# Kernel optimization log

Hardware: AMD Instinct MI355X
Metric: run time of the kernel (lower is better)

The kernel has to match this reference:

```python
import jax, jax.numpy as jnp
import numpy as np

B, S, IN_DIM, OUT_DIM = 16, 1024, 1024, 1024
NEG_SLOPE = 0.01  # torch F.leaky_relu default


def setup_inputs() -> dict:
    key = jax.random.key(0)
    ks = jax.random.split(key, 10)
    sc_in = 1.0 / np.sqrt(IN_DIM)
    sc_out = 1.0 / np.sqrt(OUT_DIM)
    return {
        "xs": jax.random.normal(ks[0], (B, S, IN_DIM), dtype=jnp.float32),
        "mask": jax.random.randint(ks[1], (B, S), 0, 2, dtype=jnp.int32),
        "Wk": jax.random.uniform(ks[2], (OUT_DIM, IN_DIM), jnp.float32, -sc_in, sc_in),
        "bk": jax.random.uniform(ks[3], (OUT_DIM,), jnp.float32, -sc_in, sc_in),
        "Wq": jax.random.uniform(ks[4], (OUT_DIM, IN_DIM), jnp.float32, -sc_in, sc_in),
        "bq": jax.random.uniform(ks[5], (OUT_DIM,), jnp.float32, -sc_in, sc_in),
        "Wv": jax.random.uniform(ks[6], (OUT_DIM, IN_DIM), jnp.float32, -sc_in, sc_in),
        "bv": jax.random.uniform(ks[7], (OUT_DIM,), jnp.float32, -sc_in, sc_in),
        "Wlin": jax.random.uniform(ks[8], (OUT_DIM, OUT_DIM), jnp.float32, -sc_out, sc_out),
        "blin": jax.random.uniform(ks[9], (OUT_DIM,), jnp.float32, -sc_out, sc_out),
    }


def reference(xs, mask, Wk, bk, Wq, bq, Wv, bv, Wlin, blin):
    # projections: torch Linear is x @ W.T + b
    K = jnp.einsum('bsi,oi->bso', xs, Wk) + bk  # [B,S,D]
    Q = jnp.einsum('bsi,oi->bso', xs, Wq) + bq  # [B,S,D]
    V = jnp.einsum('bsi,oi->bso', xs, Wv) + bv  # [B,S,D]
    # qk[b,s,e] = sum_d K[b,s,d] * Q[b,e,d]
    qk = jnp.einsum('bsd,bed->bse', K, Q) / xs.shape[-1]
    # mask.repeat(1,S).view(B,S,S) => element [b,i,j] = mask[b,j] (column/key mask)
    qk = jnp.where(mask[:, None, :].astype(bool), qk, -jnp.inf)
    a = jax.nn.softmax(qk, axis=-1)  # [B,S,S]
    # faithful to einsum('bij,bik->bik'): sum a over last axis, scale V elementwise
    attn = jnp.sum(a, axis=-1, keepdims=True) * V  # [B,S,D]
    out = jnp.einsum('bsd,od->bso', attn, Wlin) + blin
    return jnp.where(out >= 0, out, NEG_SLOPE * out)
```

## Files before the change

### kernel.cpp

```cpp
#include <hip/hip_runtime.h>
#include <hip/hip_bf16.h>
#include <stdint.h>


#define M_TOT 16384
#define KDIM  1024
#define NDIM  1024
#define NT    32

typedef __attribute__((ext_vector_type(8))) short bf16x8;
typedef __attribute__((ext_vector_type(4))) float f32x4;
typedef __attribute__((ext_vector_type(4))) unsigned short u16x4;
typedef __attribute__((ext_vector_type(8))) unsigned short u16x8;

static __device__ __forceinline__ unsigned short f2bf(float f) {
    union { float f; unsigned int u; } v; v.f = f;
    unsigned int u = v.u;
    return (unsigned short)((u + 0x7fffu + ((u >> 16) & 1u)) >> 16);
}

static __device__ __forceinline__ void gload16(const void* g, void* l) {
    __builtin_amdgcn_global_load_lds(
        (__attribute__((address_space(1))) void*)(g),
        (__attribute__((address_space(3))) void*)(l), 16, 0, 0);
}

static __device__ __forceinline__ int swz(int p) {
    return p ^ (((p >> 9) & 1) << 5) ^ (((p >> 8) & 1) << 4);
}

__global__ __launch_bounds__(256) void prep0_kernel(
    const float* __restrict__ Wv, const float* __restrict__ Wlin,
    const float* __restrict__ bv, const float* __restrict__ blin,
    unsigned short* __restrict__ Wvt, unsigned short* __restrict__ Wlb,
    float* __restrict__ bcomb) {
    __shared__ float Tl[64 * 65];
    const int bid = blockIdx.x;
    const int t = threadIdx.x;

    if (bid < 256) {
        const int dt = bid >> 4;
        const int it = bid & 15;
        const int r = t >> 2;
        const int c0 = (t & 3) * 16;
        #pragma unroll
        for (int u = 0; u < 4; ++u) {
            float4 v = *(const float4*)&Wv[((size_t)(dt * 64 + r)) * NDIM + it * 64 + c0 + 4 * u];
            Tl[r * 65 + c0 + 4 * u + 0] = v.x;
            Tl[r * 65 + c0 + 4 * u + 1] = v.y;
            Tl[r * 65 + c0 + 4 * u + 2] = v.z;
            Tl[r * 65 + c0 + 4 * u + 3] = v.w;
        }
        __syncthreads();
        const int i = t >> 2;
        const int dq = (t & 3) * 16;
        float v[16];
        #pragma unroll
        for (int u = 0; u < 16; ++u) v[u] = Tl[(dq + u) * 65 + i];
        u16x8 p0 = { f2bf(v[0]), f2bf(v[1]), f2bf(v[2]), f2bf(v[3]),
                     f2bf(v[4]), f2bf(v[5]), f2bf(v[6]), f2bf(v[7]) };
        u16x8 p1 = { f2bf(v[8]), f2bf(v[9]), f2bf(v[10]), f2bf(v[11]),
                     f2bf(v[12]), f2bf(v[13]), f2bf(v[14]), f2bf(v[15]) };
        unsigned short* dst = &Wvt[((size_t)(it * 64 + i)) * KDIM + dt * 64 + dq];
        *(u16x8*)dst = p0;
        *(u16x8*)(dst + 8) = p1;
    } else if (bid < 512) {
        const size_t idx = (((size_t)(bid - 256)) * 256 + t) * 16;
        float4 a = *(const float4*)&Wlin[idx];
        float4 b = *(const float4*)&Wlin[idx + 4];
        float4 c = *(const float4*)&Wlin[idx + 8];
        float4 d = *(const float4*)&Wlin[idx + 12];
        u16x8 p0 = { f2bf(a.x), f2bf(a.y), f2bf(a.z), f2bf(a.w),
                     f2bf(b.x), f2bf(b.y), f2bf(b.z), f2bf(b.w) };
        u16x8 p1 = { f2bf(c.x), f2bf(c.y), f2bf(c.z), f2bf(c.w),
                     f2bf(d.x), f2bf(d.y), f2bf(d.z), f2bf(d.w) };
        *(u16x8*)&Wlb[idx] = p0;
        *(u16x8*)&Wlb[idx + 8] = p1;
    } else {
        const int wave = t >> 6, lane = t & 63;
        const int o = (bid - 512) * 4 + wave;
        float s = 0.f;
        for (int d = lane; d < KDIM; d += 64) s += Wlin[o * KDIM + d] * bv[d];
        #pragma unroll
        for (int off = 32; off > 0; off >>= 1) s += __shfl_down(s, off, 64);
        if (lane == 0) bcomb[o] = s + blin[o];
    }
}

__global__ __launch_bounds__(256) void prep1_kernel(
    const unsigned short* __restrict__ Wlb, const unsigned short* __restrict__ Wvt,
    const float* __restrict__ xs, unsigned short* __restrict__ Wc,
    unsigned short* __restrict__ Xb) {
    __shared__ unsigned short As[128 * 32];
    __shared__ unsigned short Bs[128 * 32];
    const int bid = blockIdx.x;
    const int t = threadIdx.x;

    if (bid >= 64) {
        const size_t base = (((size_t)(bid - 64)) * 256 + t) * 8;
        #pragma unroll
        for (int itr = 0; itr < 4; ++itr) {
            const size_t idx = base + (size_t)itr * (size_t)(2048 * 256 * 8);
            float4 a = *(const float4*)&xs[idx];
            float4 b = *(const float4*)&xs[idx + 4];
            u16x8 p = { f2bf(a.x), f2bf(a.y), f2bf(a.z), f2bf(a.w),
                        f2bf(b.x), f2bf(b.y), f2bf(b.z), f2bf(b.w) };
            *(u16x8*)&Xb[idx] = p;
        }
        return;
    }

    const int nt8 = bid & 7;
    const int mt8 = bid >> 3;
    const int w = t >> 6, l = t & 63;
    const int wr = (w >> 1) * 64, wcc = (w & 1) * 64;
    const int lr = l & 15, lk = l >> 4;

    f32x4 acc[4][4] = {};

    const int srow = t >> 2;
    const int sc8 = (t & 3) * 8;
    const unsigned short* gA = &Wlb[((size_t)(mt8 * 128) + srow) * KDIM + sc8];
    const unsigned short* gB = &Wvt[((size_t)(nt8 * 128) + srow) * KDIM + sc8];
    unsigned short* lA0 = &As[w * 512];
    unsigned short* lB0 = &Bs[w * 512];

    for (int kt = 0; kt < KDIM / 32; ++kt) {
        #pragma unroll
        for (int j = 0; j < 2; ++j) {
            gload16(gA + (size_t)j * 64 * KDIM + kt * 32, lA0 + j * 2048);
            gload16(gB + (size_t)j * 64 * KDIM + kt * 32, lB0 + j * 2048);
        }
        __syncthreads();
        bf16x8 af[4], bfr[4];
        #pragma unroll
        for (int fi = 0; fi < 4; ++fi)
            af[fi] = *(bf16x8*)&As[(wr + fi * 16 + lr) * 32 + lk * 8];
        #pragma unroll
        for (int fj = 0; fj < 4; ++fj)
            bfr[fj] = *(bf16x8*)&Bs[(wcc + fj * 16 + lr) * 32 + lk * 8];
        #pragma unroll
        for (int fi = 0; fi < 4; ++fi)
            #pragma unroll
            for (int fj = 0; fj < 4; ++fj)
                acc[fi][fj] = __builtin_amdgcn_mfma_f32_16x16x32_bf16(
                    af[fi], bfr[fj], acc[fi][fj], 0, 0, 0);
        __syncthreads();
    }

    #pragma unroll
    for (int fi = 0; fi < 4; ++fi)
        #pragma unroll
        for (int fj = 0; fj < 4; ++fj) {
            const int col = nt8 * 128 + wcc + fj * 16 + lr;
            #pragma unroll
            for (int r = 0; r < 4; ++r) {
                const int row = mt8 * 128 + wr + fi * 16 + lk * 4 + r;
                Wc[(size_t)row * KDIM + col] = f2bf(acc[fi][fj][r]);
            }
        }
}

__global__ __launch_bounds__(512, 2) void main_gemm_8p(
    const unsigned short* __restrict__ Xb, const unsigned short* __restrict__ Wc,
    const float* __restrict__ bcomb, float* __restrict__ out) {
    extern __shared__ char lds[];
    const int tid = threadIdx.x;
    const int w = tid >> 6, l = tid & 63;
    const int wm = w >> 2, wn = w & 3;
    const int lr = l & 15, lk = l >> 4;

    const int swzb = ((blockIdx.x & 7) << 5) + (blockIdx.x >> 3);
    const int mt = swzb >> 2, nt = swzb & 3;

    int aoff[8], boff[4];
    #pragma unroll
    for (int fi = 0; fi < 8; ++fi)
        aoff[fi] = swz((wm * 128 + fi * 16 + lr) * 64 + lk * 16);
    #pragma unroll
    for (int fj = 0; fj < 4; ++fj)
        boff[fj] = 16384 + swz((wn * 64 + fj * 16 + lr) * 64 + lk * 16);

    const char* srcA0; const char* srcA1; const char* srcB0; const char* srcB1;
    {
        int q0 = 0 * 8192 + w * 1024 + l * 16, p0 = swz(q0);
        int q1 = 1 * 8192 + w * 1024 + l * 16, p1 = swz(q1);
        srcA0 = (const char*)Xb + ((size_t)(mt * 256 + (p0 >> 6)) * KDIM) * 2 + (p0 & 63);
        srcA1 = (const char*)Xb + ((size_t)(mt * 256 + (p1 >> 6)) * KDIM) * 2 + (p1 & 63);
        srcB0 = (const char*)Wc + ((size_t)(nt * 256 + (p0 >> 6)) * KDIM) * 2 + (p0 & 63);
        srcB1 = (const char*)Wc + ((size_t)(nt * 256 + (p1 >> 6)) * KDIM) * 2 + (p1 & 63);
    }
    const int ldsw = w * 1024;

    f32x4 acc[8][4] = {};

    #pragma unroll
    for (int pt = 0; pt < 3; ++pt) {
        char* bb = lds + pt * 32768;
        gload16(srcA0 + (size_t)pt * 64, bb + ldsw);
        gload16(srcA1 + (size_t)pt * 64, bb + 8192 + ldsw);
        gload16(srcB0 + (size_t)pt * 64, bb + 16384 + ldsw);
        gload16(srcB1 + (size_t)pt * 64, bb + 24576 + ldsw);
    }

#define KTILE(T, STAGE_EN)                                                     \
    do {                                                                       \
        const char* bufp = lds + (size_t)((T) & 3) * 32768;                    \
        char* nb = lds + (size_t)(((T) + 3) & 3) * 32768;                      \
        if (STAGE_EN) {                                                        \
            gload16(srcA0 + (size_t)((T) + 3) * 64, nb + ldsw);                \
            gload16(srcA1 + (size_t)((T) + 3) * 64, nb + 8192 + ldsw);         \
        }                                                                      \
        bf16x8 bfr[4], afr[4];                                                 \
        _Pragma("unroll")                                                      \
        for (int fj = 0; fj < 4; ++fj)                                         \
            bfr[fj] = *(const bf16x8*)(bufp + boff[fj]);                       \
        _Pragma("unroll")                                                      \
        for (int fi = 0; fi < 4; ++fi)                                         \
            afr[fi] = *(const bf16x8*)(bufp + aoff[fi]);                       \
        __builtin_amdgcn_s_barrier();                                          \
        __builtin_amdgcn_s_setprio(1);                                         \
        _Pragma("unroll")                                                      \
        for (int fi = 0; fi < 4; ++fi)                                         \
            _Pragma("unroll")                                                  \
            for (int fj = 0; fj < 4; ++fj)                                     \
                acc[fi][fj] = __builtin_amdgcn_mfma_f32_16x16x32_bf16(         \
                    afr[fi], bfr[fj], acc[fi][fj], 0, 0, 0);                   \
        __builtin_amdgcn_s_setprio(0);                                         \
        __builtin_amdgcn_s_barrier();                                          \
        if (STAGE_EN) {                                                        \
            gload16(srcB0 + (size_t)((T) + 3) * 64, nb + 16384 + ldsw);        \
            gload16(srcB1 + (size_t)((T) + 3) * 64, nb + 24576 + ldsw);        \
        }                                                                      \
        bf16x8 af2[4];                                                         \
        _Pragma("unroll")                                                      \
        for (int fi = 0; fi < 4; ++fi)                                         \
            af2[fi] = *(const bf16x8*)(bufp + aoff[4 + fi]);                   \
        __builtin_amdgcn_s_barrier();                                          \
        __builtin_amdgcn_s_setprio(1);                                         \
        _Pragma("unroll")                                                      \
        for (int fi = 0; fi < 4; ++fi)                                         \
            _Pragma("unroll")                                                  \
            for (int fj = 0; fj < 4; ++fj)                                     \
                acc[4 + fi][fj] = __builtin_amdgcn_mfma_f32_16x16x32_bf16(     \
                    af2[fi], bfr[fj], acc[4 + fi][fj], 0, 0, 0);               \
        __builtin_amdgcn_s_setprio(0);                                         \
    } while (0)

    for (int t = 0; t < NT - 3; ++t) {
        asm volatile("s_waitcnt vmcnt(8)" ::: "memory");
        __builtin_amdgcn_s_barrier();
        KTILE(t, 1);
    }
    asm volatile("s_waitcnt vmcnt(8)" ::: "memory");
    __builtin_amdgcn_s_barrier();
    KTILE(29, 0);
    asm volatile("s_waitcnt vmcnt(4)" ::: "memory");
    __builtin_amdgcn_s_barrier();
    KTILE(30, 0);
    asm volatile("s_waitcnt vmcnt(0)" ::: "memory");
    __builtin_amdgcn_s_barrier();
    KTILE(31, 0);
#undef KTILE

    #pragma unroll
    for (int fi = 0; fi < 8; ++fi)
        #pragma unroll
        for (int fj = 0; fj < 4; ++fj) {
            const int col = nt * 256 + wn * 64 + fj * 16 + lr;
            const float b = bcomb[col];
            #pragma unroll
            for (int r = 0; r < 4; ++r) {
                const int row = mt * 256 + wm * 128 + fi * 16 + lk * 4 + r;
                float v = acc[fi][fj][r] + b;
                out[(size_t)row * NDIM + col] = v >= 0.f ? v : 0.01f * v;
            }
        }
}

__global__ __launch_bounds__(256) void main_gemm_f32(
    const float* __restrict__ X, const unsigned short* __restrict__ Wc,
    const float* __restrict__ bcomb, float* __restrict__ out) {
    __shared__ unsigned short As[128 * 32];
    __shared__ unsigned short Bs[128 * 32];
    const int t = threadIdx.x;
    const int nt = blockIdx.x & 7;
    const int mt = blockIdx.x >> 3;
    const int w = t >> 6, l = t & 63;
    const int wr = (w >> 1) * 64, wcc = (w & 1) * 64;
    const int lr = l & 15, lk = l >> 4;

    f32x4 acc[4][4] = {};

    const int arow = t >> 3;
    const int akq = t & 7;
    const int brow = t >> 2;
    const int bc4 = t & 3;

    for (int kt = 0; kt < KDIM / 32; ++kt) {
        float4 av[4];
        #pragma unroll
        for (int j = 0; j < 4; ++j) {
            const int row = j * 32 + arow;
            av[j] = *(const float4*)&X[(mt * 128 + row) * KDIM + kt * 32 + akq * 4];
        }
        __syncthreads();
        #pragma unroll
        for (int j = 0; j < 4; ++j) {
            const int row = j * 32 + arow;
            u16x4 p = { f2bf(av[j].x), f2bf(av[j].y), f2bf(av[j].z), f2bf(av[j].w) };
            *(u16x4*)&As[row * 32 + akq * 4] = p;
        }
        #pragma unroll
        for (int j = 0; j < 2; ++j) {
            const int row = j * 64 + brow;
            const unsigned short* g = &Wc[(nt * 128 + row) * KDIM + kt * 32 + bc4 * 8];
            unsigned short* ldst = &Bs[(j * 256 + w * 64) * 8];
            gload16(g, ldst);
        }
        __syncthreads();
        bf16x8 af[4], bfr[4];
        #pragma unroll
        for (int fi = 0; fi < 4; ++fi)
            af[fi] = *(bf16x8*)&As[(wr + fi * 16 + lr) * 32 + lk * 8];
        #pragma unroll
        for (int fj = 0; fj < 4; ++fj)
            bfr[fj] = *(bf16x8*)&Bs[(wcc + fj * 16 + lr) * 32 + lk * 8];
        #pragma unroll
        for (int fi = 0; fi < 4; ++fi)
            #pragma unroll
            for (int fj = 0; fj < 4; ++fj)
                acc[fi][fj] = __builtin_amdgcn_mfma_f32_16x16x32_bf16(
                    af[fi], bfr[fj], acc[fi][fj], 0, 0, 0);
    }

    #pragma unroll
    for (int fi = 0; fi < 4; ++fi)
        #pragma unroll
        for (int fj = 0; fj < 4; ++fj) {
            const int col = nt * 128 + wcc + fj * 16 + lr;
            const float b = bcomb[col];
            #pragma unroll
            for (int r = 0; r < 4; ++r) {
                const int row = mt * 128 + wr + fi * 16 + lk * 4 + r;
                float v = acc[fi][fj][r] + b;
                out[row * NDIM + col] = v >= 0.f ? v : 0.01f * v;
            }
        }
}

extern "C" void kernel_launch(void* const* d_in, const int* in_sizes, int n_in,
                              void* d_out, int out_size, void* d_ws, size_t ws_size,
                              hipStream_t stream) {
    const float* xs   = (const float*)d_in[0];
    const float* Wv   = (const float*)d_in[6];
    const float* bv   = (const float*)d_in[7];
    const float* Wlin = (const float*)d_in[8];
    const float* blin = (const float*)d_in[9];

    unsigned short* Wc = (unsigned short*)d_ws;
    float* bcomb = (float*)((char*)d_ws + 2097152);
    unsigned short* Xb = (unsigned short*)((char*)d_ws + 2101248);
    float* out = (float*)d_out;

    unsigned short* Wvt = (unsigned short*)d_out;
    unsigned short* Wlb = (unsigned short*)((char*)d_out + 2097152);

    const size_t NEED = 2101248 + (size_t)M_TOT * KDIM * 2;
    if (ws_size >= NEED) {
        (void)hipFuncSetAttribute((const void*)main_gemm_8p,
                                  hipFuncAttributeMaxDynamicSharedMemorySize,
                                  131072);
        hipLaunchKernelGGL(prep0_kernel, dim3(768), dim3(256), 0, stream,
                           Wv, Wlin, bv, blin, Wvt, Wlb, bcomb);
        hipLaunchKernelGGL(prep1_kernel, dim3(64 + 2048), dim3(256), 0, stream,
                           Wlb, Wvt, xs, Wc, Xb);
        hipLaunchKernelGGL(main_gemm_8p, dim3(256), dim3(512), 131072, stream,
                           Xb, Wc, bcomb, out);
    } else {
        hipLaunchKernelGGL(prep0_kernel, dim3(768), dim3(256), 0, stream,
                           Wv, Wlin, bv, blin, Wvt, Wlb, bcomb);
        hipLaunchKernelGGL(prep1_kernel, dim3(64), dim3(256), 0, stream,
                           Wlb, Wvt, xs, Wc, Xb);
        hipLaunchKernelGGL(main_gemm_f32, dim3((M_TOT / 128) * (NDIM / 128)),
                           dim3(256), 0, stream, xs, Wc, bcomb, out);
    }
}
```

Measured before the change: 83.10 us.

## Fuse fp32-to-bf16 conversion of xs into main GEMM A-tile loading

```diff
diff --git a/kernel.cpp b/kernel.cpp
--- a/kernel.cpp
+++ b/kernel.cpp
@@ -6,7 +6,7 @@
 #define M_TOT 16384
 #define KDIM  1024
 #define NDIM  1024
-#define NT    32
+#define NKT   16
 
 typedef __attribute__((ext_vector_type(8))) short bf16x8;
 typedef __attribute__((ext_vector_type(4))) float f32x4;
@@ -19,14 +19,20 @@
     return (unsigned short)((u + 0x7fffu + ((u >> 16) & 1u)) >> 16);
 }
 
+static __device__ __forceinline__ u16x8 pack8(float4 a, float4 b) {
+    u16x8 p = { f2bf(a.x), f2bf(a.y), f2bf(a.z), f2bf(a.w),
+                f2bf(b.x), f2bf(b.y), f2bf(b.z), f2bf(b.w) };
+    return p;
+}
+
 static __device__ __forceinline__ void gload16(const void* g, void* l) {
     __builtin_amdgcn_global_load_lds(
         (__attribute__((address_space(1))) void*)(g),
         (__attribute__((address_space(3))) void*)(l), 16, 0, 0);
 }
 
-static __device__ __forceinline__ int swz(int p) {
-    return p ^ (((p >> 9) & 1) << 5) ^ (((p >> 8) & 1) << 4);
+static __device__ __forceinline__ int swz128(int p) {
+    return p ^ (((p >> 7) & 7) << 4);
 }
 
 __global__ __launch_bounds__(256) void prep0_kernel(
@@ -70,12 +76,8 @@
         float4 b = *(const float4*)&Wlin[idx + 4];
         float4 c = *(const float4*)&Wlin[idx + 8];
         float4 d = *(const float4*)&Wlin[idx + 12];
-        u16x8 p0 = { f2bf(a.x), f2bf(a.y), f2bf(a.z), f2bf(a.w),
-                     f2bf(b.x), f2bf(b.y), f2bf(b.z), f2bf(b.w) };
-        u16x8 p1 = { f2bf(c.x), f2bf(c.y), f2bf(c.z), f2bf(c.w),
-                     f2bf(d.x), f2bf(d.y), f2bf(d.z), f2bf(d.w) };
-        *(u16x8*)&Wlb[idx] = p0;
-        *(u16x8*)&Wlb[idx + 8] = p1;
+        *(u16x8*)&Wlb[idx] = pack8(a, b);
+        *(u16x8*)&Wlb[idx + 8] = pack8(c, d);
     } else {
         const int wave = t >> 6, lane = t & 63;
         const int o = (bid - 512) * 4 + wave;
@@ -87,82 +89,58 @@
     }
 }
 
-__global__ __launch_bounds__(256) void prep1_kernel(
+__global__ __launch_bounds__(256) void wcomb_kernel(
     const unsigned short* __restrict__ Wlb, const unsigned short* __restrict__ Wvt,
-    const float* __restrict__ xs, unsigned short* __restrict__ Wc,
-    unsigned short* __restrict__ Xb) {
-    __shared__ unsigned short As[128 * 32];
-    __shared__ unsigned short Bs[128 * 32];
-    const int bid = blockIdx.x;
+    unsigned short* __restrict__ Wc) {
+    __shared__ unsigned short As[64 * 32];
+    __shared__ unsigned short Bs[64 * 32];
     const int t = threadIdx.x;
-
-    if (bid >= 64) {
-        const size_t base = (((size_t)(bid - 64)) * 256 + t) * 8;
-        #pragma unroll
-        for (int itr = 0; itr < 4; ++itr) {
-            const size_t idx = base + (size_t)itr * (size_t)(2048 * 256 * 8);
-            float4 a = *(const float4*)&xs[idx];
-            float4 b = *(const float4*)&xs[idx + 4];
-            u16x8 p = { f2bf(a.x), f2bf(a.y), f2bf(a.z), f2bf(a.w),
-                        f2bf(b.x), f2bf(b.y), f2bf(b.z), f2bf(b.w) };
-            *(u16x8*)&Xb[idx] = p;
-        }
-        return;
-    }
-
-    const int nt8 = bid & 7;
-    const int mt8 = bid >> 3;
+    const int ot = blockIdx.x >> 4;
+    const int it = blockIdx.x & 15;
     const int w = t >> 6, l = t & 63;
-    const int wr = (w >> 1) * 64, wcc = (w & 1) * 64;
+    const int wr = (w >> 1) * 32, wc = (w & 1) * 32;
     const int lr = l & 15, lk = l >> 4;
 
-    f32x4 acc[4][4] = {};
-
-    const int srow = t >> 2;
-    const int sc8 = (t & 3) * 8;
-    const unsigned short* gA = &Wlb[((size_t)(mt8 * 128) + srow) * KDIM + sc8];
-    const unsigned short* gB = &Wvt[((size_t)(nt8 * 128) + srow) * KDIM + sc8];
-    unsigned short* lA0 = &As[w * 512];
-    unsigned short* lB0 = &Bs[w * 512];
+    f32x4 acc[2][2] = {};
+
+    const unsigned short* gA = &Wlb[((size_t)(ot * 64 + (t >> 2))) * KDIM + (t & 3) * 8];
+    const unsigned short* gB = &Wvt[((size_t)(it * 64 + (t >> 2))) * KDIM + (t & 3) * 8];
+    unsigned short* lA = &As[w * 512];
+    unsigned short* lB = &Bs[w * 512];
 
     for (int kt = 0; kt < KDIM / 32; ++kt) {
-        #pragma unroll
-        for (int j = 0; j < 2; ++j) {
-            gload16(gA + (size_t)j * 64 * KDIM + kt * 32, lA0 + j * 2048);
-            gload16(gB + (size_t)j * 64 * KDIM + kt * 32, lB0 + j * 2048);
-        }
+        gload16(gA + kt * 32, lA);
+        gload16(gB + kt * 32, lB);
         __syncthreads();
-        bf16x8 af[4], bfr[4];
-        #pragma unroll
-        for (int fi = 0; fi < 4; ++fi)
+        bf16x8 af[2], bfr[2];
+        #pragma unroll
+        for (int fi = 0; fi < 2; ++fi)
             af[fi] = *(bf16x8*)&As[(wr + fi * 16 + lr) * 32 + lk * 8];
         #pragma unroll
-        for (int fj = 0; fj < 4; ++fj)
-            bfr[fj] = *(bf16x8*)&Bs[(wcc + fj * 16 + lr) * 32 + lk * 8];
-        #pragma unroll
-        for (int fi = 0; fi < 4; ++fi)
+        for (int fj = 0; fj < 2; ++fj)
+            bfr[fj] = *(bf16x8*)&Bs[(wc + fj * 16 + lr) * 32 + lk * 8];
+        #pragma unroll
+        for (int fi = 0; fi < 2; ++fi)
             #pragma unroll
-            for (int fj = 0; fj < 4; ++fj)
+            for (int fj = 0; fj < 2; ++fj)
                 acc[fi][fj] = __builtin_amdgcn_mfma_f32_16x16x32_bf16(
                     af[fi], bfr[fj], acc[fi][fj], 0, 0, 0);
         __syncthreads();
     }
-
-    #pragma unroll
-    for (int fi = 0; fi < 4; ++fi)
-        #pragma unroll
-        for (int fj = 0; fj < 4; ++fj) {
-            const int col = nt8 * 128 + wcc + fj * 16 + lr;
+    #pragma unroll
+    for (int fi = 0; fi < 2; ++fi)
+        #pragma unroll
+        for (int fj = 0; fj < 2; ++fj)
             #pragma unroll
             for (int r = 0; r < 4; ++r) {
-                const int row = mt8 * 128 + wr + fi * 16 + lk * 4 + r;
-                Wc[(size_t)row * KDIM + col] = f2bf(acc[fi][fj][r]);
+                const int o = ot * 64 + wr + fi * 16 + lk * 4 + r;
+                const int i = it * 64 + wc + fj * 16 + lr;
+                Wc[(size_t)o * KDIM + i] = f2bf(acc[fi][fj][r]);
             }
-        }
-}
-
-__global__ __launch_bounds__(512, 2) void main_gemm_8p(
-    const unsigned short* __restrict__ Xb, const unsigned short* __restrict__ Wc,
+}
+
+__global__ __launch_bounds__(512, 2) void main_fused(
+    const float* __restrict__ xs, const unsigned short* __restrict__ Wc,
     const float* __restrict__ bcomb, float* __restrict__ out) {
     extern __shared__ char lds[];
     const int tid = threadIdx.x;
@@ -176,92 +154,146 @@
     int aoff[8], boff[4];
     #pragma unroll
     for (int fi = 0; fi < 8; ++fi)
-        aoff[fi] = swz((wm * 128 + fi * 16 + lr) * 64 + lk * 16);
+        aoff[fi] = swz128((wm * 128 + fi * 16 + lr) * 128 + lk * 16);
     #pragma unroll
     for (int fj = 0; fj < 4; ++fj)
-        boff[fj] = 16384 + swz((wn * 64 + fj * 16 + lr) * 64 + lk * 16);
-
-    const char* srcA0; const char* srcA1; const char* srcB0; const char* srcB1;
+        boff[fj] = 32768 + swz128((wn * 64 + fj * 16 + lr) * 128 + lk * 16);
+
+    const float* gA[4];
+    int awr[4];
+    #pragma unroll
+    for (int j = 0; j < 4; ++j) {
+        const int row = j * 64 + (tid >> 3);
+        gA[j] = xs + ((size_t)(mt * 256 + row)) * KDIM + (tid & 7) * 8;
+        awr[j] = swz128(row * 128 + (tid & 7) * 16);
+    }
+    const char* gB[4];
+    #pragma unroll
+    for (int j = 0; j < 4; ++j) {
+        const int q = j * 8192 + w * 1024 + l * 16;
+        const int p = swz128(q);
+        gB[j] = (const char*)Wc + ((size_t)(nt * 256 + (p >> 7))) * 2048 + (p & 127);
+    }
+    const int bofs[4] = { 32768 + w * 1024, 32768 + 8192 + w * 1024,
+                          32768 + 16384 + w * 1024, 32768 + 24576 + w * 1024 };
+
+    f32x4 acc[8][4] = {};
+
     {
-        int q0 = 0 * 8192 + w * 1024 + l * 16, p0 = swz(q0);
-        int q1 = 1 * 8192 + w * 1024 + l * 16, p1 = swz(q1);
-        srcA0 = (const char*)Xb + ((size_t)(mt * 256 + (p0 >> 6)) * KDIM) * 2 + (p0 & 63);
-        srcA1 = (const char*)Xb + ((size_t)(mt * 256 + (p1 >> 6)) * KDIM) * 2 + (p1 & 63);
-        srcB0 = (const char*)Wc + ((size_t)(nt * 256 + (p0 >> 6)) * KDIM) * 2 + (p0 & 63);
-        srcB1 = (const char*)Wc + ((size_t)(nt * 256 + (p1 >> 6)) * KDIM) * 2 + (p1 & 63);
-    }
-    const int ldsw = w * 1024;
-
-    f32x4 acc[8][4] = {};
-
-    #pragma unroll
-    for (int pt = 0; pt < 3; ++pt) {
-        char* bb = lds + pt * 32768;
-        gload16(srcA0 + (size_t)pt * 64, bb + ldsw);
-        gload16(srcA1 + (size_t)pt * 64, bb + 8192 + ldsw);
-        gload16(srcB0 + (size_t)pt * 64, bb + 16384 + ldsw);
-        gload16(srcB1 + (size_t)pt * 64, bb + 24576 + ldsw);
-    }
-
-#define KTILE(T, STAGE_EN)                                                     \
+        float4 av[8];
+        #pragma unroll
+        for (int j = 0; j < 4; ++j) {
+            av[2 * j]     = *(const float4*)(gA[j]);
+            av[2 * j + 1] = *(const float4*)(gA[j] + 4);
+        }
+        #pragma unroll
+        for (int j = 0; j < 4; ++j)
+            gload16(gB[j], lds + bofs[j]);
+        #pragma unroll
+        for (int j = 0; j < 4; ++j)
+            *(u16x8*)(lds + awr[j]) = pack8(av[2 * j], av[2 * j + 1]);
+        asm volatile("s_waitcnt vmcnt(0)" ::: "memory");
+        asm volatile("s_waitcnt lgkmcnt(0)" ::: "memory");
+        __builtin_amdgcn_s_barrier();
+    }
+
+#define MFMA16(ACCI, AF, BF)                                                   \
+    _Pragma("unroll")                                                          \
+    for (int fi = 0; fi < 4; ++fi)                                             \
+        _Pragma("unroll")                                                      \
+        for (int fj = 0; fj < 4; ++fj)                                         \
+            acc[(ACCI) + fi][fj] = __builtin_amdgcn_mfma_f32_16x16x32_bf16(    \
+                (AF)[fi], (BF)[fj], acc[(ACCI) + fi][fj], 0, 0, 0)
+
+#define PH_SYNC()                                                              \
+    __builtin_amdgcn_s_barrier();                                              \
+    asm volatile("s_waitcnt lgkmcnt(0)" ::: "memory");                         \
+    __builtin_amdgcn_sched_barrier(0)
+
+#define ITER(T, SEN)                                                           \
     do {                                                                       \
-        const char* bufp = lds + (size_t)((T) & 3) * 32768;                    \
-        char* nb = lds + (size_t)(((T) + 3) & 3) * 32768;                      \
-        if (STAGE_EN) {                                                        \
-            gload16(srcA0 + (size_t)((T) + 3) * 64, nb + ldsw);                \
-            gload16(srcA1 + (size_t)((T) + 3) * 64, nb + 8192 + ldsw);         \
+        const int cb = ((T) & 1) << 16;                                        \
+        char* cbuf = lds + cb;                                                 \
+        char* nbuf = lds + (cb ^ 65536);                                       \
+        float4 av[8];                                                          \
+        if (SEN) {                                                             \
+            _Pragma("unroll")                                                  \
+            for (int j = 0; j < 4; ++j) {                                      \
+                av[2 * j]     = *(const float4*)(gA[j] + ((T) + 1) * 64);      \
+                av[2 * j + 1] = *(const float4*)(gA[j] + ((T) + 1) * 64 + 4);  \
+            }                                                                  \
+            gload16(gB[0] + ((size_t)(T) + 1) * 128, nbuf + bofs[0]);          \
+            gload16(gB[1] + ((size_t)(T) + 1) * 128, nbuf + bofs[1]);          \
         }                                                                      \
-        bf16x8 bfr[4], afr[4];                                                 \
+                                               \
+        bf16x8 b0[4], a0[4];                                                   \
         _Pragma("unroll")                                                      \
         for (int fj = 0; fj < 4; ++fj)                                         \
-            bfr[fj] = *(const bf16x8*)(bufp + boff[fj]);                       \
+            b0[fj] = *(const bf16x8*)(cbuf + boff[fj]);                        \
         _Pragma("unroll")                                                      \
         for (int fi = 0; fi < 4; ++fi)                                         \
-            afr[fi] = *(const bf16x8*)(bufp + aoff[fi]);                       \
-        __builtin_amdgcn_s_barrier();                                          \
+            a0[fi] = *(const bf16x8*)(cbuf + aoff[fi]);                        \
+        PH_SYNC();                                                             \
         __builtin_amdgcn_s_setprio(1);                                         \
-        _Pragma("unroll")                                                      \
-        for (int fi = 0; fi < 4; ++fi)                                         \
-            _Pragma("unroll")                                                  \
-            for (int fj = 0; fj < 4; ++fj)                                     \
-                acc[fi][fj] = __builtin_amdgcn_mfma_f32_16x16x32_bf16(         \
-                    afr[fi], bfr[fj], acc[fi][fj], 0, 0, 0);                   \
+        MFMA16(0, a0, b0);                                                     \
         __builtin_amdgcn_s_setprio(0);                                         \
         __builtin_amdgcn_s_barrier();                                          \
-        if (STAGE_EN) {                                                        \
-            gload16(srcB0 + (size_t)((T) + 3) * 64, nb + 16384 + ldsw);        \
-            gload16(srcB1 + (size_t)((T) + 3) * 64, nb + 24576 + ldsw);        \
+                    \
+        bf16x8 a1[4];                                                          \
+        _Pragma("unroll")                                                      \
+        for (int fi = 0; fi < 4; ++fi)                                         \
+            a1[fi] = *(const bf16x8*)(cbuf + aoff[4 + fi]);                    \
+        if (SEN) {                                                             \
+            *(u16x8*)(nbuf + awr[0]) = pack8(av[0], av[1]);                    \
+            *(u16x8*)(nbuf + awr[1]) = pack8(av[2], av[3]);                    \
+            gload16(gB[2] + ((size_t)(T) + 1) * 128, nbuf + bofs[2]);          \
+            gload16(gB[3] + ((size_t)(T) + 1) * 128, nbuf + bofs[3]);          \
         }                                                                      \
-        bf16x8 af2[4];                                                         \
+        PH_SYNC();                                                             \
+        __builtin_amdgcn_s_setprio(1);                                         \
+        MFMA16(4, a1, b0);                                                     \
+        __builtin_amdgcn_s_setprio(0);                                         \
+        __builtin_amdgcn_s_barrier();                                          \
+                         \
+        bf16x8 b1[4], a2[4];                                                   \
+        _Pragma("unroll")                                                      \
+        for (int fj = 0; fj < 4; ++fj)                                         \
+            b1[fj] = *(const bf16x8*)(cbuf + (boff[fj] ^ 64));                 \
         _Pragma("unroll")                                                      \
         for (int fi = 0; fi < 4; ++fi)                                         \
-            af2[fi] = *(const bf16x8*)(bufp + aoff[4 + fi]);                   \
+            a2[fi] = *(const bf16x8*)(cbuf + (aoff[fi] ^ 64));                 \
+        if (SEN) {                                                             \
+            *(u16x8*)(nbuf + awr[2]) = pack8(av[4], av[5]);                    \
+            *(u16x8*)(nbuf + awr[3]) = pack8(av[6], av[7]);                    \
+        }                                                                      \
+        PH_SYNC();                                                             \
+        __builtin_amdgcn_s_setprio(1);                                         \
+        MFMA16(0, a2, b1);                                                     \
+        __builtin_amdgcn_s_setprio(0);                                         \
         __builtin_amdgcn_s_barrier();                                          \
+                                                       \
+        bf16x8 a3[4];                                                          \
+        _Pragma("unroll")                                                      \
+        for (int fi = 0; fi < 4; ++fi)                                         \
+            a3[fi] = *(const bf16x8*)(cbuf + (aoff[4 + fi] ^ 64));             \
+        PH_SYNC();                                                             \
         __builtin_amdgcn_s_setprio(1);                                         \
-        _Pragma("unroll")                                                      \
-        for (int fi = 0; fi < 4; ++fi)                                         \
-            _Pragma("unroll")                                                  \
-            for (int fj = 0; fj < 4; ++fj)                                     \
-                acc[4 + fi][fj] = __builtin_amdgcn_mfma_f32_16x16x32_bf16(     \
-                    af2[fi], bfr[fj], acc[4 + fi][fj], 0, 0, 0);               \
+        MFMA16(4, a3, b1);                                                     \
         __builtin_amdgcn_s_setprio(0);                                         \
+        if (SEN) {                                                             \
+            asm volatile("s_waitcnt vmcnt(0)" ::: "memory");                   \
+            asm volatile("s_waitcnt lgkmcnt(0)" ::: "memory");                 \
+            __builtin_amdgcn_s_barrier();                                      \
+        }                                                                      \
     } while (0)
 
-    for (int t = 0; t < NT - 3; ++t) {
-        asm volatile("s_waitcnt vmcnt(8)" ::: "memory");
-        __builtin_amdgcn_s_barrier();
-        KTILE(t, 1);
-    }
-    asm volatile("s_waitcnt vmcnt(8)" ::: "memory");
-    __builtin_amdgcn_s_barrier();
-    KTILE(29, 0);
-    asm volatile("s_waitcnt vmcnt(4)" ::: "memory");
-    __builtin_amdgcn_s_barrier();
-    KTILE(30, 0);
-    asm volatile("s_waitcnt vmcnt(0)" ::: "memory");
-    __builtin_amdgcn_s_barrier();
-    KTILE(31, 0);
-#undef KTILE
+    for (int T = 0; T < NKT - 1; ++T) {
+        ITER(T, 1);
+    }
+    ITER(NKT - 1, 0);
+#undef ITER
+#undef PH_SYNC
+#undef MFMA16
 
     #pragma unroll
     for (int fi = 0; fi < 8; ++fi)
@@ -360,28 +392,23 @@
 
     unsigned short* Wc = (unsigned short*)d_ws;
     float* bcomb = (float*)((char*)d_ws + 2097152);
-    unsigned short* Xb = (unsigned short*)((char*)d_ws + 2101248);
     float* out = (float*)d_out;
 
     unsigned short* Wvt = (unsigned short*)d_out;
     unsigned short* Wlb = (unsigned short*)((char*)d_out + 2097152);
 
-    const size_t NEED = 2101248 + (size_t)M_TOT * KDIM * 2;
+    const size_t NEED = 2101248;
+    hipLaunchKernelGGL(prep0_kernel, dim3(768), dim3(256), 0, stream,
+                       Wv, Wlin, bv, blin, Wvt, Wlb, bcomb);
+    hipLaunchKernelGGL(wcomb_kernel, dim3(256), dim3(256), 0, stream,
+                       Wlb, Wvt, Wc);
     if (ws_size >= NEED) {
-        (void)hipFuncSetAttribute((const void*)main_gemm_8p,
+        (void)hipFuncSetAttribute((const void*)main_fused,
                                   hipFuncAttributeMaxDynamicSharedMemorySize,
                                   131072);
-        hipLaunchKernelGGL(prep0_kernel, dim3(768), dim3(256), 0, stream,
-                           Wv, Wlin, bv, blin, Wvt, Wlb, bcomb);
-        hipLaunchKernelGGL(prep1_kernel, dim3(64 + 2048), dim3(256), 0, stream,
-                           Wlb, Wvt, xs, Wc, Xb);
-        hipLaunchKernelGGL(main_gemm_8p, dim3(256), dim3(512), 131072, stream,
-                           Xb, Wc, bcomb, out);
+        hipLaunchKernelGGL(main_fused, dim3(256), dim3(512), 131072, stream,
+                           xs, Wc, bcomb, out);
     } else {
-        hipLaunchKernelGGL(prep0_kernel, dim3(768), dim3(256), 0, stream,
-                           Wv, Wlin, bv, blin, Wvt, Wlb, bcomb);
-        hipLaunchKernelGGL(prep1_kernel, dim3(64), dim3(256), 0, stream,
-                           Wlb, Wvt, xs, Wc, Xb);
         hipLaunchKernelGGL(main_gemm_f32, dim3((M_TOT / 128) * (NDIM / 128)),
                            dim3(256), 0, stream, xs, Wc, bcomb, out);
     }
```

Result: faster. 79.98 us (-3.8%).

## Shrink weight-fold GEMM tiles and switch main GEMM LDS to 128-byte swizzle

Applied to the files above, without the earlier changes.

```diff
diff --git a/kernel.cpp b/kernel.cpp
--- a/kernel.cpp
+++ b/kernel.cpp
@@ -19,14 +19,20 @@
     return (unsigned short)((u + 0x7fffu + ((u >> 16) & 1u)) >> 16);
 }
 
+static __device__ __forceinline__ u16x8 pack8(float4 a, float4 b) {
+    u16x8 p = { f2bf(a.x), f2bf(a.y), f2bf(a.z), f2bf(a.w),
+                f2bf(b.x), f2bf(b.y), f2bf(b.z), f2bf(b.w) };
+    return p;
+}
+
 static __device__ __forceinline__ void gload16(const void* g, void* l) {
     __builtin_amdgcn_global_load_lds(
         (__attribute__((address_space(1))) void*)(g),
         (__attribute__((address_space(3))) void*)(l), 16, 0, 0);
 }
 
-static __device__ __forceinline__ int swz(int p) {
-    return p ^ (((p >> 9) & 1) << 5) ^ (((p >> 8) & 1) << 4);
+static __device__ __forceinline__ int swz128(int p) {
+    return p ^ (((p >> 7) & 7) << 4);
 }
 
 __global__ __launch_bounds__(256) void prep0_kernel(
@@ -70,12 +76,8 @@
         float4 b = *(const float4*)&Wlin[idx + 4];
         float4 c = *(const float4*)&Wlin[idx + 8];
         float4 d = *(const float4*)&Wlin[idx + 12];
-        u16x8 p0 = { f2bf(a.x), f2bf(a.y), f2bf(a.z), f2bf(a.w),
-                     f2bf(b.x), f2bf(b.y), f2bf(b.z), f2bf(b.w) };
-        u16x8 p1 = { f2bf(c.x), f2bf(c.y), f2bf(c.z), f2bf(c.w),
-                     f2bf(d.x), f2bf(d.y), f2bf(d.z), f2bf(d.w) };
-        *(u16x8*)&Wlb[idx] = p0;
-        *(u16x8*)&Wlb[idx + 8] = p1;
+        *(u16x8*)&Wlb[idx] = pack8(a, b);
+        *(u16x8*)&Wlb[idx + 8] = pack8(c, d);
     } else {
         const int wave = t >> 6, lane = t & 63;
         const int o = (bid - 512) * 4 + wave;
@@ -91,77 +93,68 @@
     const unsigned short* __restrict__ Wlb, const unsigned short* __restrict__ Wvt,
     const float* __restrict__ xs, unsigned short* __restrict__ Wc,
     unsigned short* __restrict__ Xb) {
-    __shared__ unsigned short As[128 * 32];
-    __shared__ unsigned short Bs[128 * 32];
+    __shared__ unsigned short As[64 * 32];
+    __shared__ unsigned short Bs[64 * 32];
     const int bid = blockIdx.x;
     const int t = threadIdx.x;
 
-    if (bid >= 64) {
-        const size_t base = (((size_t)(bid - 64)) * 256 + t) * 8;
+    if (bid >= 256) {
+        const size_t base = (((size_t)(bid - 256)) * 256 + t) * 8;
         #pragma unroll
         for (int itr = 0; itr < 4; ++itr) {
             const size_t idx = base + (size_t)itr * (size_t)(2048 * 256 * 8);
             float4 a = *(const float4*)&xs[idx];
             float4 b = *(const float4*)&xs[idx + 4];
-            u16x8 p = { f2bf(a.x), f2bf(a.y), f2bf(a.z), f2bf(a.w),
-                        f2bf(b.x), f2bf(b.y), f2bf(b.z), f2bf(b.w) };
-            *(u16x8*)&Xb[idx] = p;
+            *(u16x8*)&Xb[idx] = pack8(a, b);
         }
         return;
     }
 
-    const int nt8 = bid & 7;
-    const int mt8 = bid >> 3;
+    const int ot = bid >> 4;
+    const int it = bid & 15;
     const int w = t >> 6, l = t & 63;
-    const int wr = (w >> 1) * 64, wcc = (w & 1) * 64;
+    const int wr = (w >> 1) * 32, wc = (w & 1) * 32;
     const int lr = l & 15, lk = l >> 4;
 
-    f32x4 acc[4][4] = {};
-
-    const int srow = t >> 2;
-    const int sc8 = (t & 3) * 8;
-    const unsigned short* gA = &Wlb[((size_t)(mt8 * 128) + srow) * KDIM + sc8];
-    const unsigned short* gB = &Wvt[((size_t)(nt8 * 128) + srow) * KDIM + sc8];
-    unsigned short* lA0 = &As[w * 512];
-    unsigned short* lB0 = &Bs[w * 512];
+    f32x4 acc[2][2] = {};
+
+    const unsigned short* gA = &Wlb[((size_t)(ot * 64 + (t >> 2))) * KDIM + (t & 3) * 8];
+    const unsigned short* gB = &Wvt[((size_t)(it * 64 + (t >> 2))) * KDIM + (t & 3) * 8];
+    unsigned short* lA = &As[w * 512];
+    unsigned short* lB = &Bs[w * 512];
 
     for (int kt = 0; kt < KDIM / 32; ++kt) {
-        #pragma unroll
-        for (int j = 0; j < 2; ++j) {
-            gload16(gA + (size_t)j * 64 * KDIM + kt * 32, lA0 + j * 2048);
-            gload16(gB + (size_t)j * 64 * KDIM + kt * 32, lB0 + j * 2048);
-        }
-        __syncthreads();
-        bf16x8 af[4], bfr[4];
-        #pragma unroll
-        for (int fi = 0; fi < 4; ++fi)
+        gload16(gA + kt * 32, lA);
+        gload16(gB + kt * 32, lB);
+        __syncthreads();
+        bf16x8 af[2], bfr[2];
+        #pragma unroll
+        for (int fi = 0; fi < 2; ++fi)
             af[fi] = *(bf16x8*)&As[(wr + fi * 16 + lr) * 32 + lk * 8];
         #pragma unroll
-        for (int fj = 0; fj < 4; ++fj)
-            bfr[fj] = *(bf16x8*)&Bs[(wcc + fj * 16 + lr) * 32 + lk * 8];
-        #pragma unroll
-        for (int fi = 0; fi < 4; ++fi)
-            #pragma unroll
-            for (int fj = 0; fj < 4; ++fj)
+        for (int fj = 0; fj < 2; ++fj)
+            bfr[fj] = *(bf16x8*)&Bs[(wc + fj * 16 + lr) * 32 + lk * 8];
+        #pragma unroll
+        for (int fi = 0; fi < 2; ++fi)
+            #pragma unroll
+            for (int fj = 0; fj < 2; ++fj)
                 acc[fi][fj] = __builtin_amdgcn_mfma_f32_16x16x32_bf16(
                     af[fi], bfr[fj], acc[fi][fj], 0, 0, 0);
         __syncthreads();
     }
-
-    #pragma unroll
-    for (int fi = 0; fi < 4; ++fi)
-        #pragma unroll
-        for (int fj = 0; fj < 4; ++fj) {
-            const int col = nt8 * 128 + wcc + fj * 16 + lr;
+    #pragma unroll
+    for (int fi = 0; fi < 2; ++fi)
+        #pragma unroll
+        for (int fj = 0; fj < 2; ++fj)
             #pragma unroll
             for (int r = 0; r < 4; ++r) {
-                const int row = mt8 * 128 + wr + fi * 16 + lk * 4 + r;
-                Wc[(size_t)row * KDIM + col] = f2bf(acc[fi][fj][r]);
+                const int o = ot * 64 + wr + fi * 16 + lk * 4 + r;
+                const int i = it * 64 + wc + fj * 16 + lr;
+                Wc[(size_t)o * KDIM + i] = f2bf(acc[fi][fj][r]);
             }
-        }
-}
-
-__global__ __launch_bounds__(512, 2) void main_gemm_8p(
+}
+
+__global__ __launch_bounds__(512, 2) void main_ring(
     const unsigned short* __restrict__ Xb, const unsigned short* __restrict__ Wc,
     const float* __restrict__ bcomb, float* __restrict__ out) {
     extern __shared__ char lds[];
@@ -175,20 +168,26 @@
 
     int aoff[8], boff[4];
     #pragma unroll
-    for (int fi = 0; fi < 8; ++fi)
-        aoff[fi] = swz((wm * 128 + fi * 16 + lr) * 64 + lk * 16);
-    #pragma unroll
-    for (int fj = 0; fj < 4; ++fj)
-        boff[fj] = 16384 + swz((wn * 64 + fj * 16 + lr) * 64 + lk * 16);
+    for (int fi = 0; fi < 8; ++fi) {
+        const int r = wm * 128 + fi * 16 + lr;
+        aoff[fi] = swz128(((r >> 1) << 7) | ((r & 1) << 6) | (lk << 4));
+    }
+    #pragma unroll
+    for (int fj = 0; fj < 4; ++fj) {
+        const int r = wn * 64 + fj * 16 + lr;
+        boff[fj] = 16384 + swz128(((r >> 1) << 7) | ((r & 1) << 6) | (lk << 4));
+    }
 
     const char* srcA0; const char* srcA1; const char* srcB0; const char* srcB1;
     {
-        int q0 = 0 * 8192 + w * 1024 + l * 16, p0 = swz(q0);
-        int q1 = 1 * 8192 + w * 1024 + l * 16, p1 = swz(q1);
-        srcA0 = (const char*)Xb + ((size_t)(mt * 256 + (p0 >> 6)) * KDIM) * 2 + (p0 & 63);
-        srcA1 = (const char*)Xb + ((size_t)(mt * 256 + (p1 >> 6)) * KDIM) * 2 + (p1 & 63);
-        srcB0 = (const char*)Wc + ((size_t)(nt * 256 + (p0 >> 6)) * KDIM) * 2 + (p0 & 63);
-        srcB1 = (const char*)Wc + ((size_t)(nt * 256 + (p1 >> 6)) * KDIM) * 2 + (p1 & 63);
+        const int q0 = 0 * 8192 + w * 1024 + l * 16, p0 = swz128(q0);
+        const int q1 = 1 * 8192 + w * 1024 + l * 16, p1 = swz128(q1);
+        const int r0 = ((p0 >> 7) << 1) | ((p0 >> 6) & 1), c0 = p0 & 63;
+        const int r1 = ((p1 >> 7) << 1) | ((p1 >> 6) & 1), c1 = p1 & 63;
+        srcA0 = (const char*)Xb + ((size_t)(mt * 256 + r0) * KDIM) * 2 + c0;
+        srcA1 = (const char*)Xb + ((size_t)(mt * 256 + r1) * KDIM) * 2 + c1;
+        srcB0 = (const char*)Wc + ((size_t)(nt * 256 + r0) * KDIM) * 2 + c0;
+        srcB1 = (const char*)Wc + ((size_t)(nt * 256 + r1) * KDIM) * 2 + c1;
     }
     const int ldsw = w * 1024;
 
@@ -207,6 +206,7 @@
     do {                                                                       \
         const char* bufp = lds + (size_t)((T) & 3) * 32768;                    \
         char* nb = lds + (size_t)(((T) + 3) & 3) * 32768;                      \
+               \
         if (STAGE_EN) {                                                        \
             gload16(srcA0 + (size_t)((T) + 3) * 64, nb + ldsw);                \
             gload16(srcA1 + (size_t)((T) + 3) * 64, nb + 8192 + ldsw);         \
@@ -228,6 +228,7 @@
                     afr[fi], bfr[fj], acc[fi][fj], 0, 0, 0);                   \
         __builtin_amdgcn_s_setprio(0);                                         \
         __builtin_amdgcn_s_barrier();                                          \
+                        \
         if (STAGE_EN) {                                                        \
             gload16(srcB0 + (size_t)((T) + 3) * 64, nb + 16384 + ldsw);        \
             gload16(srcB1 + (size_t)((T) + 3) * 64, nb + 24576 + ldsw);        \
@@ -367,20 +368,18 @@
     unsigned short* Wlb = (unsigned short*)((char*)d_out + 2097152);
 
     const size_t NEED = 2101248 + (size_t)M_TOT * KDIM * 2;
+    hipLaunchKernelGGL(prep0_kernel, dim3(768), dim3(256), 0, stream,
+                       Wv, Wlin, bv, blin, Wvt, Wlb, bcomb);
     if (ws_size >= NEED) {
-        (void)hipFuncSetAttribute((const void*)main_gemm_8p,
+        (void)hipFuncSetAttribute((const void*)main_ring,
                                   hipFuncAttributeMaxDynamicSharedMemorySize,
                                   131072);
-        hipLaunchKernelGGL(prep0_kernel, dim3(768), dim3(256), 0, stream,
-                           Wv, Wlin, bv, blin, Wvt, Wlb, bcomb);
-        hipLaunchKernelGGL(prep1_kernel, dim3(64 + 2048), dim3(256), 0, stream,
+        hipLaunchKernelGGL(prep1_kernel, dim3(256 + 2048), dim3(256), 0, stream,
                            Wlb, Wvt, xs, Wc, Xb);
-        hipLaunchKernelGGL(main_gemm_8p, dim3(256), dim3(512), 131072, stream,
+        hipLaunchKernelGGL(main_ring, dim3(256), dim3(512), 131072, stream,
                            Xb, Wc, bcomb, out);
     } else {
-        hipLaunchKernelGGL(prep0_kernel, dim3(768), dim3(256), 0, stream,
-                           Wv, Wlin, bv, blin, Wvt, Wlb, bcomb);
-        hipLaunchKernelGGL(prep1_kernel, dim3(64), dim3(256), 0, stream,
+        hipLaunchKernelGGL(prep1_kernel, dim3(256), dim3(256), 0, stream,
                            Wlb, Wvt, xs, Wc, Xb);
         hipLaunchKernelGGL(main_gemm_f32, dim3((M_TOT / 128) * (NDIM / 128)),
                            dim3(256), 0, stream, xs, Wc, bcomb, out);
```

New measurement: 74.92 us. -9.8%, faster.
